# Kernel optimization log

Hardware: AMD Instinct MI355X
Metric: run time of the kernel (lower is better)

The kernel has to match this reference:

```python
import jax, jax.numpy as jnp
import numpy as np

N, M, D = 20000, 16000, 128

def setup_inputs() -> dict:
    key = jax.random.key(0)
    ks = jax.random.split(key, 4)
    return {
        "clear_feature": jax.random.normal(ks[0], (N, D), dtype=jnp.float32),
        "rain_feature": jax.random.normal(ks[1], (M, D), dtype=jnp.float32),
        # torch nn.Linear weight layout: (out_features, in_features)
        "W1": jax.random.normal(ks[2], (D, 2 * D), dtype=jnp.float32) * 0.05,
        "b1": jnp.zeros((D,), dtype=jnp.float32),
        "W2": jax.random.normal(ks[3], (1, D), dtype=jnp.float32) * 0.05,
        "b2": jnp.zeros((1,), dtype=jnp.float32),
    }

def reference(clear_feature, rain_feature, W1, b1, W2, b2):
    # --- KNN alignment (k=1): argmin of squared Euclidean distance == cdist+topk(smallest) ---
    x2 = jnp.sum(clear_feature * clear_feature, axis=-1, keepdims=True)   # [N,1]
    y2 = jnp.sum(rain_feature * rain_feature, axis=-1)                    # [M]
    d2 = x2 + y2 - 2.0 * (clear_feature @ rain_feature.T)                 # [N,M]
    idx = jnp.argmin(d2, axis=-1)                                         # [N]
    aligned = rain_feature[idx]                                           # [N,D] gather
    # --- attention MLP: Linear(2D->D) + ReLU + Linear(D->1) + Sigmoid ---
    comb = jnp.concatenate([clear_feature, aligned], axis=-1)             # [N,2D]
    h = jax.nn.relu(comb @ W1.T + b1)                                     # [N,D]
    w = jax.nn.sigmoid(h @ W2.T + b2)                                     # [N,1]
    # --- gated fusion ---
    return w * clear_feature + (1.0 - w) * aligned
```

## Files before the change

kernel.cpp:

```cpp
#include <hip/hip_runtime.h>
#include <stdint.h>

#define NN 20000
#define MM 16000
#define DD 128
#define CT2 250
#define SPLITS 32
#define RB 79

typedef unsigned long long u64;
typedef _Float16 f16x8 __attribute__((ext_vector_type(8)));
typedef float f32x16 __attribute__((ext_vector_type(16)));

__global__ void k_prep(const float* __restrict__ rain, const float* __restrict__ W1,
                       float* __restrict__ y2, _Float16* __restrict__ Bimg,
                       _Float16* __restrict__ W1img) {
    const int bb = blockIdx.x;
    const int tid = threadIdx.x;
    if (bb < 4000) {
        int row = bb * 4 + (tid >> 6);
        int lane = tid & 63;
        if (row >= MM) return;
        float2 v = ((const float2*)(rain + (size_t)row * DD))[lane];
        float s = v.x * v.x + v.y * v.y;
        #pragma unroll
        for (int off = 32; off > 0; off >>= 1) s += __shfl_down(s, off);
        if (lane == 0) y2[row] = s;
    } else if (bb < 5000) {
        int id = (bb - 4000) * 256 + tid;
        int cl = id & 31;
        int cg = (id >> 5) & 1;
        int kp = (id >> 6) & 15;
        int tc = id >> 10;
        int row = tc * 64 + cg * 32 + cl;
        const float4* src = (const float4*)(rain + (size_t)row * DD + kp * 8);
        float4 v0 = src[0], v1 = src[1];
        float x[8] = {v0.x, v0.y, v0.z, v0.w, v1.x, v1.y, v1.z, v1.w};
        _Float16 hi[8], lo[8];
        #pragma unroll
        for (int j = 0; j < 8; ++j) {
            _Float16 h = (_Float16)x[j];
            hi[j] = h;
            lo[j] = (_Float16)(x[j] - (float)h);
        }
        int ks = kp >> 1, kh = kp & 1;
        int chunk = ((ks * 2 + cg) * 2 + kh) * 32 + cl;
        size_t base = (size_t)tc * 16384;
        *(f16x8*)(Bimg + base + (size_t)chunk * 8) = *(f16x8*)hi;
        *(f16x8*)(Bimg + base + 8192 + (size_t)chunk * 8) = *(f16x8*)lo;
    } else {
        int id = (bb - 5000) * 256 + tid;
        if (id >= 4096) return;
        int cl = id & 31;
        int kh = (id >> 5) & 1;
        int cg = (id >> 6) & 3;
        int ks = id >> 8;
        int d = cg * 32 + cl;
        int k = ks * 16 + kh * 8;
        const float4* src = (const float4*)(W1 + (size_t)d * 256 + k);
        float4 v0 = src[0], v1 = src[1];
        float x[8] = {v0.x, v0.y, v0.z, v0.w, v1.x, v1.y, v1.z, v1.w};
        _Float16 h[8];
        #pragma unroll
        for (int j = 0; j < 8; ++j) h[j] = (_Float16)x[j];
        *(f16x8*)(W1img + (size_t)id * 8) = *(f16x8*)h;
    }
}

__global__ __launch_bounds__(256, 2) void k_dist(
        const float* __restrict__ clear_f,
        const _Float16* __restrict__ Bimg, const float* __restrict__ y2,
        u64* __restrict__ keys2) {
    __shared__ _Float16 lds[2][16384];
    __shared__ float y2s[512];

    const int tid = threadIdx.x;
    const int w = tid >> 6, lane = tid & 63;
    const int l5 = lane >> 5, l31 = lane & 31;
    const int b = blockIdx.x;
    const int split = b & 31;
    const int n0 = (b >> 5) * 256;
    const int nt = (CT2 - split + SPLITS - 1) / SPLITS;

    {
        const _Float16* gsrc = Bimg + (size_t)split * 16384;
        #pragma unroll
        for (int n = 0; n < 8; ++n) {
            int seg = w * 8 + n;
            __builtin_amdgcn_global_load_lds(
                (const __attribute__((address_space(1))) unsigned int*)
                    (gsrc + (size_t)seg * 512 + (size_t)lane * 8),
                (__attribute__((address_space(3))) unsigned int*)
                    (&lds[0][0] + (size_t)seg * 512),
                16, 0, 0);
        }
    }

    for (int j = tid; j < nt * 64; j += 256) {
        int tt = j >> 6;
        int cc = j & 63;
        y2s[j] = y2[(split + tt * SPLITS) * 64 + cc];
    }

    f16x8 afh[2][8], afl[2][8];
    #pragma unroll
    for (int rb = 0; rb < 2; ++rb) {
        int r = n0 + w * 64 + rb * 32 + l31;
        if (r >= NN) r = NN - 1;
        const float* ap = clear_f + (size_t)r * DD + l5 * 8;
        #pragma unroll
        for (int ks = 0; ks < 8; ++ks) {
            float4 v0 = *(const float4*)(ap + ks * 16);
            float4 v1 = *(const float4*)(ap + ks * 16 + 4);
            float x[8] = {v0.x, v0.y, v0.z, v0.w, v1.x, v1.y, v1.z, v1.w};
            _Float16 hi[8], lo[8];
            #pragma unroll
            for (int j = 0; j < 8; ++j) {
                float s = -2.f * x[j];
                _Float16 h = (_Float16)s;
                hi[j] = h;
                lo[j] = (_Float16)(s - (float)h);
            }
            afh[rb][ks] = *(f16x8*)hi;
            afl[rb][ks] = *(f16x8*)lo;
        }
    }

    __syncthreads();

    float bestd[32];
    unsigned bits[4] = {0u, 0u, 0u, 0u};
    #pragma unroll
    for (int s = 0; s < 32; ++s) bestd[s] = 1e30f;

    int p = 0;
    for (int i = 0; i < nt; ++i) {
        const int t = split + i * SPLITS;

        if (i + 1 < nt) {
            const _Float16* gsrc = Bimg + (size_t)(t + SPLITS) * 16384;
            _Float16* dst = &lds[1 - p][0];
            #pragma unroll
            for (int n = 0; n < 8; ++n) {
                int seg = w * 8 + n;
                __builtin_amdgcn_global_load_lds(
                    (const __attribute__((address_space(1))) unsigned int*)
                        (gsrc + (size_t)seg * 512 + (size_t)lane * 8),
                    (__attribute__((address_space(3))) unsigned int*)
                        (dst + (size_t)seg * 512),
                    16, 0, 0);
            }
        }

        float y2v0 = y2s[i * 64 + l31];
        float y2v1 = y2s[i * 64 + 32 + l31];

        f32x16 acc00, acc01, acc10, acc11;
        #pragma unroll
        for (int e = 0; e < 16; ++e) {
            acc00[e] = y2v0; acc10[e] = y2v0;
            acc01[e] = y2v1; acc11[e] = y2v1;
        }

        const _Float16* lbuf = &lds[p][0];
        #pragma unroll
        for (int ks = 0; ks < 8; ++ks) {
            f16x8 bh0 = *(const f16x8*)(lbuf + (size_t)(ks * 2 + 0) * 512 + (size_t)lane * 8);
            f16x8 bh1 = *(const f16x8*)(lbuf + (size_t)(ks * 2 + 1) * 512 + (size_t)lane * 8);
            f16x8 bl0 = *(const f16x8*)(lbuf + 8192 + (size_t)(ks * 2 + 0) * 512 + (size_t)lane * 8);
            f16x8 bl1 = *(const f16x8*)(lbuf + 8192 + (size_t)(ks * 2 + 1) * 512 + (size_t)lane * 8);
            acc00 = __builtin_amdgcn_mfma_f32_32x32x16_f16(afh[0][ks], bh0, acc00, 0, 0, 0);
            acc10 = __builtin_amdgcn_mfma_f32_32x32x16_f16(afh[1][ks], bh0, acc10, 0, 0, 0);
            acc01 = __builtin_amdgcn_mfma_f32_32x32x16_f16(afh[0][ks], bh1, acc01, 0, 0, 0);
            acc11 = __builtin_amdgcn_mfma_f32_32x32x16_f16(afh[1][ks], bh1, acc11, 0, 0, 0);
            acc00 = __builtin_amdgcn_mfma_f32_32x32x16_f16(afh[0][ks], bl0, acc00, 0, 0, 0);
            acc10 = __builtin_amdgcn_mfma_f32_32x32x16_f16(afh[1][ks], bl0, acc10, 0, 0, 0);
            acc01 = __builtin_amdgcn_mfma_f32_32x32x16_f16(afh[0][ks], bl1, acc01, 0, 0, 0);
            acc11 = __builtin_amdgcn_mfma_f32_32x32x16_f16(afh[1][ks], bl1, acc11, 0, 0, 0);
            acc00 = __builtin_amdgcn_mfma_f32_32x32x16_f16(afl[0][ks], bh0, acc00, 0, 0, 0);
            acc10 = __builtin_amdgcn_mfma_f32_32x32x16_f16(afl[1][ks], bh0, acc10, 0, 0, 0);
            acc01 = __builtin_amdgcn_mfma_f32_32x32x16_f16(afl[0][ks], bh1, acc01, 0, 0, 0);
            acc11 = __builtin_amdgcn_mfma_f32_32x32x16_f16(afl[1][ks], bh1, acc11, 0, 0, 0);
        }

        const unsigned ibase = (unsigned)i << 1;
        #pragma unroll
        for (int e = 0; e < 16; ++e) {
            {
                float d0 = acc00[e], d1 = acc01[e];
                bool tk = d1 < d0;
                float dm = tk ? d1 : d0;
                int s = e, sh = 4 * (e & 7);
                bool up = dm < bestd[s];
                bestd[s] = up ? dm : bestd[s];
                unsigned nib = ibase | (unsigned)tk;
                bits[s >> 3] = up ? ((bits[s >> 3] & ~(15u << sh)) | (nib << sh))
                                  : bits[s >> 3];
            }
            {
                float d0 = acc10[e], d1 = acc11[e];
                bool tk = d1 < d0;
                float dm = tk ? d1 : d0;
                int s = 16 + e, sh = 4 * (s & 7);
                bool up = dm < bestd[s];
                bestd[s] = up ? dm : bestd[s];
                unsigned nib = ibase | (unsigned)tk;
                bits[s >> 3] = up ? ((bits[s >> 3] & ~(15u << sh)) | (nib << sh))
                                  : bits[s >> 3];
            }
        }

        __syncthreads();
        p ^= 1;
    }

    #pragma unroll
    for (int s = 0; s < 32; ++s) {
        unsigned nib = (bits[s >> 3] >> (4 * (s & 7))) & 15u;
        int i4 = (int)(nib >> 1), cg = (int)(nib & 1);
        int col = (split + i4 * SPLITS) * 64 + cg * 32 + l31;
        unsigned u = __float_as_uint(bestd[s]);
        u = (u & 0x80000000u) ? ~u : (u | 0x80000000u);
        u64 key = ((u64)u << 32) | (unsigned)col;
        #pragma unroll
        for (int off = 1; off < 32; off <<= 1) {
            u64 o = __shfl_xor(key, off);
            if (o < key) key = o;
        }
        if (l31 == 0) {
            int e = s & 15, rb = s >> 4;
            int grow = n0 + w * 64 + rb * 32 + (e & 3) + 8 * (e >> 2) + 4 * l5;
            if (grow < NN) keys2[(size_t)grow * SPLITS + split] = key;
        }
    }
}

__global__ __launch_bounds__(64) void k_mlp(
        const float* __restrict__ clear_f, const float* __restrict__ rain_f,
        const _Float16* __restrict__ W1img, const float* __restrict__ b1,
        const float* __restrict__ W2, const float* __restrict__ b2,
        const u64* __restrict__ keys2, float* __restrict__ out) {
    __shared__ int idxs[32];

    const int lane = threadIdx.x;
    const int l5 = lane >> 5, l31 = lane & 31;
    const int n0 = blockIdx.x * 32;

    {
        int r = lane >> 1;
        const u64* pk = keys2 + (size_t)(n0 + r) * SPLITS + (lane & 1) * 16;
        u64 best = pk[0];
        #pragma unroll
        for (int t = 1; t < 16; ++t) {
            u64 k2 = pk[t];
            if (k2 < best) best = k2;
        }
        u64 o = __shfl_xor(best, 1);
        if (o < best) best = o;
        if ((lane & 1) == 0) idxs[r] = (int)(best & 0xffffffffu);
    }
    __syncthreads();

    int nc = n0 + l31;
    int rid = idxs[l31];
    f16x8 af[16];
    #pragma unroll
    for (int ks = 0; ks < 16; ++ks) {
        int k0 = ks * 16 + l5 * 8;
        const float4* src = (k0 < 128)
            ? (const float4*)(clear_f + (size_t)nc * DD + k0)
            : (const float4*)(rain_f + (size_t)rid * DD + (k0 - 128));
        float4 v0 = src[0], v1 = src[1];
        float x[8] = {v0.x, v0.y, v0.z, v0.w, v1.x, v1.y, v1.z, v1.w};
        _Float16 h[8];
        #pragma unroll
        for (int j = 0; j < 8; ++j) h[j] = (_Float16)x[j];
        af[ks] = *(f16x8*)h;
    }

    f32x16 acc[4];
    #pragma unroll
    for (int cg = 0; cg < 4; ++cg)
        #pragma unroll
        for (int e = 0; e < 16; ++e) acc[cg][e] = 0.f;

    #pragma unroll
    for (int ks = 0; ks < 16; ++ks) {
        #pragma unroll
        for (int cg = 0; cg < 4; ++cg) {
            f16x8 bh = *(const f16x8*)(W1img +
                ((size_t)((ks * 4 + cg) * 2 + l5)) * 256 + (size_t)l31 * 8);
            acc[cg] = __builtin_amdgcn_mfma_f32_32x32x16_f16(af[ks], bh, acc[cg], 0, 0, 0);
        }
    }

    float b1v[4], w2v[4];
    #pragma unroll
    for (int cg = 0; cg < 4; ++cg) {
        b1v[cg] = b1[cg * 32 + l31];
        w2v[cg] = W2[cg * 32 + l31];
    }
    float b2v = b2[0];

    #pragma unroll
    for (int e = 0; e < 16; ++e) {
        float part = 0.f;
        #pragma unroll
        for (int cg = 0; cg < 4; ++cg) {
            float hv = acc[cg][e] + b1v[cg];
            hv = hv > 0.f ? hv : 0.f;
            part = fmaf(hv, w2v[cg], part);
        }
        #pragma unroll
        for (int off = 1; off < 32; off <<= 1) part += __shfl_xor(part, off);
        float s = part + b2v;
        float wv = 1.f / (1.f + expf(-s));
        int row = n0 + (e & 3) + 8 * (e >> 2) + 4 * l5;
        int rid2 = idxs[row - n0];
        float4 cv = *(const float4*)(clear_f + (size_t)row * DD + l31 * 4);
        float4 av = *(const float4*)(rain_f + (size_t)rid2 * DD + l31 * 4);
        float4 ov;
        ov.x = wv * cv.x + (1.f - wv) * av.x;
        ov.y = wv * cv.y + (1.f - wv) * av.y;
        ov.z = wv * cv.z + (1.f - wv) * av.z;
        ov.w = wv * cv.w + (1.f - wv) * av.w;
        *(float4*)(out + (size_t)row * DD + l31 * 4) = ov;
    }
}

extern "C" void kernel_launch(void* const* d_in, const int* in_sizes, int n_in,
                              void* d_out, int out_size, void* d_ws, size_t ws_size,
                              hipStream_t stream) {
    const float* clear_f = (const float*)d_in[0];
    const float* rain_f = (const float*)d_in[1];
    const float* W1 = (const float*)d_in[2];
    const float* b1 = (const float*)d_in[3];
    const float* W2 = (const float*)d_in[4];
    const float* b2 = (const float*)d_in[5];
    float* out = (float*)d_out;

    char* ws = (char*)d_ws;
    u64* keys2 = (u64*)ws;
    float* y2 = (float*)(ws + 5120000);
    _Float16* Bimg = (_Float16*)(ws + 5184000);
    _Float16* W1img = (_Float16*)(ws + 13376000);

    k_prep<<<5016, 256, 0, stream>>>(rain_f, W1, y2, Bimg, W1img);
    k_dist<<<RB * SPLITS, 256, 0, stream>>>(clear_f, Bimg, y2, keys2);
    k_mlp<<<NN / 32, 64, 0, stream>>>(clear_f, rain_f, W1img, b1, W2, b2, keys2, out);
}
```

Baseline: 342.1 us.

## Split MLP K-dimension across waves with LDS reduction in k_mlp

The MLP kernel moves from one 64-thread wave per 32 rows to 256-thread blocks handling 64 rows. Each pair of waves splits the 256-wide K dimension in half (clear vs aligned features) and exchanges partial accumulators through shared memory. Each wave then finishes the bias, ReLU, dot product, sigmoid and gated output for half of the row groups. The aim is more parallelism and shorter per-wave MFMA chains in the MLP stage, at the cost of an LDS round-trip, an extra barrier and bounds checks for the padded last block.

```diff
diff --git a/kernel.cpp b/kernel.cpp
--- a/kernel.cpp
+++ b/kernel.cpp
@@ -235,47 +235,52 @@
     }
 }
 
-__global__ __launch_bounds__(64) void k_mlp(
+__global__ __launch_bounds__(256) void k_mlp(
         const float* __restrict__ clear_f, const float* __restrict__ rain_f,
         const _Float16* __restrict__ W1img, const float* __restrict__ b1,
         const float* __restrict__ W2, const float* __restrict__ b2,
         const u64* __restrict__ keys2, float* __restrict__ out) {
-    __shared__ int idxs[32];
-
-    const int lane = threadIdx.x;
+    __shared__ int idxs[64];
+    __shared__ float comb[2][2][64][32];
+
+    const int tid = threadIdx.x;
+    const int w = tid >> 6, lane = tid & 63;
     const int l5 = lane >> 5, l31 = lane & 31;
-    const int n0 = blockIdx.x * 32;
+    const int pr = w >> 1, kh = w & 1;
+    const int n0 = blockIdx.x * 64;
 
     {
-        int r = lane >> 1;
-        const u64* pk = keys2 + (size_t)(n0 + r) * SPLITS + (lane & 1) * 16;
+        int r = tid >> 2, q = tid & 3;
+        int rr = n0 + r; if (rr >= NN) rr = NN - 1;
+        const u64* pk = keys2 + (size_t)rr * SPLITS + q * 8;
         u64 best = pk[0];
         #pragma unroll
-        for (int t = 1; t < 16; ++t) {
+        for (int t = 1; t < 8; ++t) {
             u64 k2 = pk[t];
             if (k2 < best) best = k2;
         }
-        u64 o = __shfl_xor(best, 1);
-        if (o < best) best = o;
-        if ((lane & 1) == 0) idxs[r] = (int)(best & 0xffffffffu);
+        u64 o = __shfl_xor(best, 1); if (o < best) best = o;
+        o = __shfl_xor(best, 2); if (o < best) best = o;
+        if (q == 0) idxs[r] = (int)(best & 0xffffffffu);
     }
     __syncthreads();
 
-    int nc = n0 + l31;
-    int rid = idxs[l31];
-    f16x8 af[16];
-    #pragma unroll
-    for (int ks = 0; ks < 16; ++ks) {
-        int k0 = ks * 16 + l5 * 8;
-        const float4* src = (k0 < 128)
-            ? (const float4*)(clear_f + (size_t)nc * DD + k0)
-            : (const float4*)(rain_f + (size_t)rid * DD + (k0 - 128));
+    int nrow = n0 + pr * 32 + l31;
+    if (nrow >= NN) nrow = NN - 1;
+    int rid = idxs[pr * 32 + l31];
+    f16x8 af[8];
+    #pragma unroll
+    for (int ksl = 0; ksl < 8; ++ksl) {
+        int k0 = ksl * 16 + l5 * 8;
+        const float4* src = (kh == 0)
+            ? (const float4*)(clear_f + (size_t)nrow * DD + k0)
+            : (const float4*)(rain_f + (size_t)rid * DD + k0);
         float4 v0 = src[0], v1 = src[1];
         float x[8] = {v0.x, v0.y, v0.z, v0.w, v1.x, v1.y, v1.z, v1.w};
         _Float16 h[8];
         #pragma unroll
         for (int j = 0; j < 8; ++j) h[j] = (_Float16)x[j];
-        af[ks] = *(f16x8*)h;
+        af[ksl] = *(f16x8*)h;
     }
 
     f32x16 acc[4];
@@ -285,13 +290,44 @@
         for (int e = 0; e < 16; ++e) acc[cg][e] = 0.f;
 
     #pragma unroll
-    for (int ks = 0; ks < 16; ++ks) {
+    for (int ksl = 0; ksl < 8; ++ksl) {
+        int ks = kh * 8 + ksl;
         #pragma unroll
         for (int cg = 0; cg < 4; ++cg) {
             f16x8 bh = *(const f16x8*)(W1img +
                 ((size_t)((ks * 4 + cg) * 2 + l5)) * 256 + (size_t)l31 * 8);
-            acc[cg] = __builtin_amdgcn_mfma_f32_32x32x16_f16(af[ks], bh, acc[cg], 0, 0, 0);
-        }
+            acc[cg] = __builtin_amdgcn_mfma_f32_32x32x16_f16(af[ksl], bh, acc[cg], 0, 0, 0);
+        }
+    }
+
+    if (kh == 0) {
+        #pragma unroll
+        for (int cg = 0; cg < 4; ++cg)
+            #pragma unroll
+            for (int eo = 0; eo < 8; ++eo)
+                comb[pr][0][lane][cg * 8 + eo] = acc[cg][8 + eo];
+    } else {
+        #pragma unroll
+        for (int cg = 0; cg < 4; ++cg)
+            #pragma unroll
+            for (int eo = 0; eo < 8; ++eo)
+                comb[pr][1][lane][cg * 8 + eo] = acc[cg][eo];
+    }
+    __syncthreads();
+
+    float hsum[4][8];
+    if (kh == 0) {
+        #pragma unroll
+        for (int cg = 0; cg < 4; ++cg)
+            #pragma unroll
+            for (int eo = 0; eo < 8; ++eo)
+                hsum[cg][eo] = acc[cg][eo] + comb[pr][1][lane][cg * 8 + eo];
+    } else {
+        #pragma unroll
+        for (int cg = 0; cg < 4; ++cg)
+            #pragma unroll
+            for (int eo = 0; eo < 8; ++eo)
+                hsum[cg][eo] = acc[cg][8 + eo] + comb[pr][0][lane][cg * 8 + eo];
     }
 
     float b1v[4], w2v[4];
@@ -303,11 +339,11 @@
     float b2v = b2[0];
 
     #pragma unroll
-    for (int e = 0; e < 16; ++e) {
+    for (int eo = 0; eo < 8; ++eo) {
         float part = 0.f;
         #pragma unroll
         for (int cg = 0; cg < 4; ++cg) {
-            float hv = acc[cg][e] + b1v[cg];
+            float hv = hsum[cg][eo] + b1v[cg];
             hv = hv > 0.f ? hv : 0.f;
             part = fmaf(hv, w2v[cg], part);
         }
@@ -315,16 +351,19 @@
         for (int off = 1; off < 32; off <<= 1) part += __shfl_xor(part, off);
         float s = part + b2v;
         float wv = 1.f / (1.f + expf(-s));
-        int row = n0 + (e & 3) + 8 * (e >> 2) + 4 * l5;
-        int rid2 = idxs[row - n0];
-        float4 cv = *(const float4*)(clear_f + (size_t)row * DD + l31 * 4);
-        float4 av = *(const float4*)(rain_f + (size_t)rid2 * DD + l31 * 4);
-        float4 ov;
-        ov.x = wv * cv.x + (1.f - wv) * av.x;
-        ov.y = wv * cv.y + (1.f - wv) * av.y;
-        ov.z = wv * cv.z + (1.f - wv) * av.z;
-        ov.w = wv * cv.w + (1.f - wv) * av.w;
-        *(float4*)(out + (size_t)row * DD + l31 * 4) = ov;
+        int e = kh * 8 + eo;
+        int row = n0 + pr * 32 + (e & 3) + 8 * (e >> 2) + 4 * l5;
+        if (row < NN) {
+            int rid2 = idxs[row - n0];
+            float4 cv = *(const float4*)(clear_f + (size_t)row * DD + l31 * 4);
+            float4 av = *(const float4*)(rain_f + (size_t)rid2 * DD + l31 * 4);
+            float4 ov;
+            ov.x = wv * cv.x + (1.f - wv) * av.x;
+            ov.y = wv * cv.y + (1.f - wv) * av.y;
+            ov.z = wv * cv.z + (1.f - wv) * av.z;
+            ov.w = wv * cv.w + (1.f - wv) * av.w;
+            *(float4*)(out + (size_t)row * DD + l31 * 4) = ov;
+        }
     }
 }
 
@@ -347,5 +386,5 @@
 
     k_prep<<<5016, 256, 0, stream>>>(rain_f, W1, y2, Bimg, W1img);
     k_dist<<<RB * SPLITS, 256, 0, stream>>>(clear_f, Bimg, y2, keys2);
-    k_mlp<<<NN / 32, 64, 0, stream>>>(clear_f, rain_f, W1img, b1, W2, b2, keys2, out);
+    k_mlp<<<(NN + 63) / 64, 256, 0, stream>>>(clear_f, rain_f, W1img, b1, W2, b2, keys2, out);
 }
```

Result: slower. 351.9 us (+2.9%).

## Triple-buffer distance kernel with 512-thread blocks and phased MFMA/prefetch interleave

Applied to the files above, without the earlier changes.

Doubles the block size of the distance kernel to 512 threads so each block covers 512 query rows and shares each staged rain tile across twice as many rows. It also switches to a three-stage LDS ring with a two-tile-ahead prefetch. Each tile's K loop is split into four phases that issue one slice of the next-next tile's async load, then run MFMAs at raised priority, with explicit waitcnt and barriers replacing __syncthreads. The intent is to hide global load latency and halve redundant rain-tile traffic, at the cost of more LDS, one block per CU and more barriers per tile.

```diff
diff --git a/kernel.cpp b/kernel.cpp
--- a/kernel.cpp
+++ b/kernel.cpp
@@ -6,7 +6,7 @@
 #define DD 128
 #define CT2 250
 #define SPLITS 32
-#define RB 79
+#define RB2 40
 
 typedef unsigned long long u64;
 typedef _Float16 f16x8 __attribute__((ext_vector_type(8)));
@@ -67,11 +67,11 @@
     }
 }
 
-__global__ __launch_bounds__(256, 2) void k_dist(
+__global__ __launch_bounds__(512, 1) void k_dist(
         const float* __restrict__ clear_f,
         const _Float16* __restrict__ Bimg, const float* __restrict__ y2,
         u64* __restrict__ keys2) {
-    __shared__ _Float16 lds[2][16384];
+    __shared__ _Float16 lds[3][16384];
     __shared__ float y2s[512];
 
     const int tid = threadIdx.x;
@@ -79,24 +79,36 @@
     const int l5 = lane >> 5, l31 = lane & 31;
     const int b = blockIdx.x;
     const int split = b & 31;
-    const int n0 = (b >> 5) * 256;
+    const int n0 = (b >> 5) * 512;
     const int nt = (CT2 - split + SPLITS - 1) / SPLITS;
 
-    {
-        const _Float16* gsrc = Bimg + (size_t)split * 16384;
-        #pragma unroll
-        for (int n = 0; n < 8; ++n) {
-            int seg = w * 8 + n;
-            __builtin_amdgcn_global_load_lds(
-                (const __attribute__((address_space(1))) unsigned int*)
-                    (gsrc + (size_t)seg * 512 + (size_t)lane * 8),
-                (__attribute__((address_space(3))) unsigned int*)
-                    (&lds[0][0] + (size_t)seg * 512),
-                16, 0, 0);
-        }
-    }
-
-    for (int j = tid; j < nt * 64; j += 256) {
+    #define STAGE4(T, BUF) do {                                                \
+        const _Float16* gsrc_ = Bimg + (size_t)(T) * 16384;                    \
+        _Float16* dst_ = &lds[BUF][0];                                         \
+        _Pragma("unroll")                                                      \
+        for (int n_ = 0; n_ < 4; ++n_) {                                       \
+            int seg_ = w * 4 + n_;                                             \
+            __builtin_amdgcn_global_load_lds(                                  \
+                (const __attribute__((address_space(1))) unsigned int*)        \
+                    (gsrc_ + (size_t)seg_ * 512 + (size_t)lane * 8),           \
+                (__attribute__((address_space(3))) unsigned int*)              \
+                    (dst_ + (size_t)seg_ * 512),                               \
+                16, 0, 0);                                                     \
+        }                                                                      \
+    } while (0)
+    #define STAGE1(GSRC, DST, SEG) do {                                        \
+        __builtin_amdgcn_global_load_lds(                                      \
+            (const __attribute__((address_space(1))) unsigned int*)            \
+                ((GSRC) + (size_t)(SEG) * 512 + (size_t)lane * 8),             \
+            (__attribute__((address_space(3))) unsigned int*)                  \
+                ((DST) + (size_t)(SEG) * 512),                                 \
+            16, 0, 0);                                                         \
+    } while (0)
+
+    STAGE4(split, 0);
+    if (nt > 1) STAGE4(split + SPLITS, 1);
+
+    for (int j = tid; j < nt * 64; j += 512) {
         int tt = j >> 6;
         int cc = j & 63;
         y2s[j] = y2[(split + tt * SPLITS) * 64 + cc];
@@ -126,7 +138,7 @@
         }
     }
 
-    __syncthreads();
+    asm volatile("s_waitcnt lgkmcnt(0)" ::: "memory");
 
     float bestd[32];
     unsigned bits[4] = {0u, 0u, 0u, 0u};
@@ -135,22 +147,19 @@
 
     int p = 0;
     for (int i = 0; i < nt; ++i) {
-        const int t = split + i * SPLITS;
-
         if (i + 1 < nt) {
-            const _Float16* gsrc = Bimg + (size_t)(t + SPLITS) * 16384;
-            _Float16* dst = &lds[1 - p][0];
-            #pragma unroll
-            for (int n = 0; n < 8; ++n) {
-                int seg = w * 8 + n;
-                __builtin_amdgcn_global_load_lds(
-                    (const __attribute__((address_space(1))) unsigned int*)
-                        (gsrc + (size_t)seg * 512 + (size_t)lane * 8),
-                    (__attribute__((address_space(3))) unsigned int*)
-                        (dst + (size_t)seg * 512),
-                    16, 0, 0);
-            }
-        }
+            asm volatile("s_waitcnt vmcnt(4)" ::: "memory");
+        } else {
+            asm volatile("s_waitcnt vmcnt(0)" ::: "memory");
+        }
+        __builtin_amdgcn_s_barrier();
+        __builtin_amdgcn_sched_barrier(0);
+
+        int p2 = p + 2; if (p2 >= 3) p2 -= 3;
+        const bool pf = (i + 2 < nt);
+        const _Float16* gsrc2 = Bimg + (size_t)(split + (i + 2) * SPLITS) * 16384;
+        _Float16* dst2 = &lds[p2][0];
+        const _Float16* lbuf = &lds[p][0];
 
         float y2v0 = y2s[i * 64 + l31];
         float y2v1 = y2s[i * 64 + 32 + l31];
@@ -162,26 +171,54 @@
             acc01[e] = y2v1; acc11[e] = y2v1;
         }
 
-        const _Float16* lbuf = &lds[p][0];
-        #pragma unroll
-        for (int ks = 0; ks < 8; ++ks) {
-            f16x8 bh0 = *(const f16x8*)(lbuf + (size_t)(ks * 2 + 0) * 512 + (size_t)lane * 8);
-            f16x8 bh1 = *(const f16x8*)(lbuf + (size_t)(ks * 2 + 1) * 512 + (size_t)lane * 8);
-            f16x8 bl0 = *(const f16x8*)(lbuf + 8192 + (size_t)(ks * 2 + 0) * 512 + (size_t)lane * 8);
-            f16x8 bl1 = *(const f16x8*)(lbuf + 8192 + (size_t)(ks * 2 + 1) * 512 + (size_t)lane * 8);
-            acc00 = __builtin_amdgcn_mfma_f32_32x32x16_f16(afh[0][ks], bh0, acc00, 0, 0, 0);
-            acc10 = __builtin_amdgcn_mfma_f32_32x32x16_f16(afh[1][ks], bh0, acc10, 0, 0, 0);
-            acc01 = __builtin_amdgcn_mfma_f32_32x32x16_f16(afh[0][ks], bh1, acc01, 0, 0, 0);
-            acc11 = __builtin_amdgcn_mfma_f32_32x32x16_f16(afh[1][ks], bh1, acc11, 0, 0, 0);
-            acc00 = __builtin_amdgcn_mfma_f32_32x32x16_f16(afh[0][ks], bl0, acc00, 0, 0, 0);
-            acc10 = __builtin_amdgcn_mfma_f32_32x32x16_f16(afh[1][ks], bl0, acc10, 0, 0, 0);
-            acc01 = __builtin_amdgcn_mfma_f32_32x32x16_f16(afh[0][ks], bl1, acc01, 0, 0, 0);
-            acc11 = __builtin_amdgcn_mfma_f32_32x32x16_f16(afh[1][ks], bl1, acc11, 0, 0, 0);
-            acc00 = __builtin_amdgcn_mfma_f32_32x32x16_f16(afl[0][ks], bh0, acc00, 0, 0, 0);
-            acc10 = __builtin_amdgcn_mfma_f32_32x32x16_f16(afl[1][ks], bh0, acc10, 0, 0, 0);
-            acc01 = __builtin_amdgcn_mfma_f32_32x32x16_f16(afl[0][ks], bh1, acc01, 0, 0, 0);
-            acc11 = __builtin_amdgcn_mfma_f32_32x32x16_f16(afl[1][ks], bh1, acc11, 0, 0, 0);
-        }
+        #define PHASE(P) do {                                                  \
+            const int ksA_ = 2 * (P), ksB_ = 2 * (P) + 1;                      \
+            f16x8 bh0a = *(const f16x8*)(lbuf + (size_t)(ksA_ * 2 + 0) * 512 + (size_t)lane * 8); \
+            f16x8 bh1a = *(const f16x8*)(lbuf + (size_t)(ksA_ * 2 + 1) * 512 + (size_t)lane * 8); \
+            f16x8 bl0a = *(const f16x8*)(lbuf + 8192 + (size_t)(ksA_ * 2 + 0) * 512 + (size_t)lane * 8); \
+            f16x8 bl1a = *(const f16x8*)(lbuf + 8192 + (size_t)(ksA_ * 2 + 1) * 512 + (size_t)lane * 8); \
+            f16x8 bh0b = *(const f16x8*)(lbuf + (size_t)(ksB_ * 2 + 0) * 512 + (size_t)lane * 8); \
+            f16x8 bh1b = *(const f16x8*)(lbuf + (size_t)(ksB_ * 2 + 1) * 512 + (size_t)lane * 8); \
+            f16x8 bl0b = *(const f16x8*)(lbuf + 8192 + (size_t)(ksB_ * 2 + 0) * 512 + (size_t)lane * 8); \
+            f16x8 bl1b = *(const f16x8*)(lbuf + 8192 + (size_t)(ksB_ * 2 + 1) * 512 + (size_t)lane * 8); \
+            if (pf) STAGE1(gsrc2, dst2, w * 4 + (P));                          \
+            __builtin_amdgcn_s_barrier();                                      \
+            asm volatile("s_waitcnt lgkmcnt(0)" ::: "memory");                 \
+            __builtin_amdgcn_sched_barrier(0);                                 \
+            __builtin_amdgcn_s_setprio(1);                                     \
+            acc00 = __builtin_amdgcn_mfma_f32_32x32x16_f16(afh[0][ksA_], bh0a, acc00, 0, 0, 0); \
+            acc10 = __builtin_amdgcn_mfma_f32_32x32x16_f16(afh[1][ksA_], bh0a, acc10, 0, 0, 0); \
+            acc01 = __builtin_amdgcn_mfma_f32_32x32x16_f16(afh[0][ksA_], bh1a, acc01, 0, 0, 0); \
+            acc11 = __builtin_amdgcn_mfma_f32_32x32x16_f16(afh[1][ksA_], bh1a, acc11, 0, 0, 0); \
+            acc00 = __builtin_amdgcn_mfma_f32_32x32x16_f16(afh[0][ksA_], bl0a, acc00, 0, 0, 0); \
+            acc10 = __builtin_amdgcn_mfma_f32_32x32x16_f16(afh[1][ksA_], bl0a, acc10, 0, 0, 0); \
+            acc01 = __builtin_amdgcn_mfma_f32_32x32x16_f16(afh[0][ksA_], bl1a, acc01, 0, 0, 0); \
+            acc11 = __builtin_amdgcn_mfma_f32_32x32x16_f16(afh[1][ksA_], bl1a, acc11, 0, 0, 0); \
+            acc00 = __builtin_amdgcn_mfma_f32_32x32x16_f16(afl[0][ksA_], bh0a, acc00, 0, 0, 0); \
+            acc10 = __builtin_amdgcn_mfma_f32_32x32x16_f16(afl[1][ksA_], bh0a, acc10, 0, 0, 0); \
+            acc01 = __builtin_amdgcn_mfma_f32_32x32x16_f16(afl[0][ksA_], bh1a, acc01, 0, 0, 0); \
+            acc11 = __builtin_amdgcn_mfma_f32_32x32x16_f16(afl[1][ksA_], bh1a, acc11, 0, 0, 0); \
+            acc00 = __builtin_amdgcn_mfma_f32_32x32x16_f16(afh[0][ksB_], bh0b, acc00, 0, 0, 0); \
+            acc10 = __builtin_amdgcn_mfma_f32_32x32x16_f16(afh[1][ksB_], bh0b, acc10, 0, 0, 0); \
+            acc01 = __builtin_amdgcn_mfma_f32_32x32x16_f16(afh[0][ksB_], bh1b, acc01, 0, 0, 0); \
+            acc11 = __builtin_amdgcn_mfma_f32_32x32x16_f16(afh[1][ksB_], bh1b, acc11, 0, 0, 0); \
+            acc00 = __builtin_amdgcn_mfma_f32_32x32x16_f16(afh[0][ksB_], bl0b, acc00, 0, 0, 0); \
+            acc10 = __builtin_amdgcn_mfma_f32_32x32x16_f16(afh[1][ksB_], bl0b, acc10, 0, 0, 0); \
+            acc01 = __builtin_amdgcn_mfma_f32_32x32x16_f16(afh[0][ksB_], bl1b, acc01, 0, 0, 0); \
+            acc11 = __builtin_amdgcn_mfma_f32_32x32x16_f16(afh[1][ksB_], bl1b, acc11, 0, 0, 0); \
+            acc00 = __builtin_amdgcn_mfma_f32_32x32x16_f16(afl[0][ksB_], bh0b, acc00, 0, 0, 0); \
+            acc10 = __builtin_amdgcn_mfma_f32_32x32x16_f16(afl[1][ksB_], bh0b, acc10, 0, 0, 0); \
+            acc01 = __builtin_amdgcn_mfma_f32_32x32x16_f16(afl[0][ksB_], bh1b, acc01, 0, 0, 0); \
+            acc11 = __builtin_amdgcn_mfma_f32_32x32x16_f16(afl[1][ksB_], bh1b, acc11, 0, 0, 0); \
+            __builtin_amdgcn_s_setprio(0);                                     \
+            __builtin_amdgcn_s_barrier();                                      \
+        } while (0)
+
+        PHASE(0);
+        PHASE(1);
+        PHASE(2);
+        PHASE(3);
+        #undef PHASE
 
         const unsigned ibase = (unsigned)i << 1;
         #pragma unroll
@@ -210,9 +247,10 @@
             }
         }
 
-        __syncthreads();
-        p ^= 1;
-    }
+        ++p; if (p == 3) p = 0;
+    }
+    #undef STAGE4
+    #undef STAGE1
 
     #pragma unroll
     for (int s = 0; s < 32; ++s) {
@@ -346,6 +384,6 @@
     _Float16* W1img = (_Float16*)(ws + 13376000);
 
     k_prep<<<5016, 256, 0, stream>>>(rain_f, W1, y2, Bimg, W1img);
-    k_dist<<<RB * SPLITS, 256, 0, stream>>>(clear_f, Bimg, y2, keys2);
+    k_dist<<<RB2 * SPLITS, 512, 0, stream>>>(clear_f, Bimg, y2, keys2);
     k_mlp<<<NN / 32, 64, 0, stream>>>(clear_f, rain_f, W1img, b1, W2, b2, keys2, out);
 }
```

Measured after the change: 429.6 us. +25.6%, slower.
